# Kernel optimization log

Measured on AMD Instinct MI355X. Metric: run time of the kernel, lower is better.

The kernel has to match this reference:

```python
import jax, jax.numpy as jnp
import numpy as np
from jax import lax

D_MODEL = 256
VOCAB = 512
D_INNER = 512          # expand=2
D_STATE = 64
D_CONV = 4
HEADDIM = 32
NHEADS = D_INNER // HEADDIM  # 16
NGROUPS = 1
CHUNK = 64
D_IN_PROJ = 2 * D_INNER + 2 * NGROUPS * D_STATE + NHEADS  # 1168
CONV_DIM = D_INNER + 2 * NGROUPS * D_STATE               # 640


def setup_inputs() -> dict:
    key = jax.random.key(0)
    ks = jax.random.split(key, 8)
    B, L = 8, 4096
    input_ids = jax.random.randint(ks[0], (B, L), 0, VOCAB)
    rn = lambda k, shp, sc: (jax.random.normal(k, shp) * sc).astype(jnp.float32)
    embed_w = rn(ks[1], (VOCAB, D_MODEL), 0.02).at[0].set(0.0)  # padding_idx=0
    in_proj_w = rn(ks[2], (D_IN_PROJ, D_MODEL), D_MODEL ** -0.5)
    conv_w = rn(ks[3], (CONV_DIM, D_CONV), 0.2)
    conv_b = jnp.zeros((CONV_DIM,), jnp.float32)
    A_log = jnp.log(jax.random.uniform(ks[4], (NHEADS,), minval=1.0, maxval=16.0)).astype(jnp.float32)
    D_skip = jnp.ones((NHEADS,), jnp.float32)
    dt0 = jax.random.uniform(ks[5], (NHEADS,), minval=1e-3, maxval=0.1)
    dt_bias = jnp.log(jnp.expm1(dt0)).astype(jnp.float32)  # inverse softplus
    gate_norm_w = jnp.ones((D_INNER,), jnp.float32)
    out_proj_w = rn(ks[6], (D_MODEL, D_INNER), D_INNER ** -0.5)
    norm_w = jnp.ones((D_MODEL,), jnp.float32)
    return dict(input_ids=input_ids, embed_w=embed_w, in_proj_w=in_proj_w,
                conv_w=conv_w, conv_b=conv_b, A_log=A_log, D_skip=D_skip,
                dt_bias=dt_bias, gate_norm_w=gate_norm_w, out_proj_w=out_proj_w,
                norm_w=norm_w)


def _rmsnorm(x, w, eps):
    return x * lax.rsqrt(jnp.mean(x * x, axis=-1, keepdims=True) + eps) * w


def _segsum(a):
    # a: (..., T) -> (..., T, T); out[q,s] = sum_{s+1..q} a, -inf above diag
    T = a.shape[-1]
    c = jnp.cumsum(a, axis=-1)
    seg = c[..., :, None] - c[..., None, :]
    mask = jnp.tril(jnp.ones((T, T), bool))
    return jnp.where(mask, seg, -jnp.inf)


def _ssd(X, A, Bm, Cm):
    # X:(b,l,h,p) already *dt ; A:(b,l,h)=dt*A_head ; Bm,Cm:(b,l,n)
    b, l, h, p = X.shape
    n = Bm.shape[-1]
    c, q = l // CHUNK, CHUNK
    X = X.reshape(b, c, q, h, p)
    A = A.reshape(b, c, q, h).transpose(0, 3, 1, 2)        # (b,h,c,q)
    Bm = Bm.reshape(b, c, q, n)
    Cm = Cm.reshape(b, c, q, n)
    A_cs = jnp.cumsum(A, axis=-1)                           # (b,h,c,q)
    Lmat = jnp.exp(_segsum(A))                              # (b,h,c,q,q)
    # intra-chunk (diagonal block) output
    Y_diag = jnp.einsum('bcqn,bckn,bhcqk,bckhp->bcqhp', Cm, Bm, Lmat, X)
    # states carried to end of each chunk
    decay_states = jnp.exp(A_cs[..., -1:] - A_cs)           # (b,h,c,q)
    states = jnp.einsum('bckn,bhck,bckhp->bchpn', Bm, decay_states, X)
    chunk_decay = jnp.exp(A_cs[..., -1])                    # (b,h,c)
    def step(hprev, inp):
        dec, st = inp
        return dec[..., None, None] * hprev + st, hprev
    _, prev = lax.scan(step, jnp.zeros((b, h, p, n), X.dtype),
                       (chunk_decay.transpose(2, 0, 1), states.transpose(1, 0, 2, 3, 4)))
    prev = prev.transpose(1, 0, 2, 3, 4)                    # (b,c,h,p,n)
    Y_off = jnp.einsum('bcqn,bchpn,bhcq->bcqhp', Cm, prev, jnp.exp(A_cs))
    return (Y_diag + Y_off).reshape(b, l, h, p)


def _mamba2(u, in_proj_w, conv_w, conv_b, A_log, D_skip, dt_bias, gate_norm_w, out_proj_w):
    B, L, _ = u.shape
    zxbcdt = u @ in_proj_w.T                                # (B,L,1168)
    z = zxbcdt[..., :D_INNER]
    xBC = zxbcdt[..., D_INNER:D_INNER + CONV_DIM]
    dt = zxbcdt[..., D_INNER + CONV_DIM:]                   # (B,L,H)
    # causal depthwise conv + silu
    xBC = lax.conv_general_dilated(xBC.transpose(0, 2, 1), conv_w[:, None, :],
                                   (1,), [(D_CONV - 1, 0)],
                                   dimension_numbers=('NCH', 'OIH', 'NCH'),
                                   feature_group_count=CONV_DIM)
    xBC = jax.nn.silu(xBC + conv_b[None, :, None]).transpose(0, 2, 1)
    x = xBC[..., :D_INNER].reshape(B, L, NHEADS, HEADDIM)
    Bm = xBC[..., D_INNER:D_INNER + D_STATE]
    Cm = xBC[..., D_INNER + D_STATE:]
    dt = jax.nn.softplus(dt + dt_bias)                      # (B,L,H)
    A = -jnp.exp(A_log)                                     # (H,)
    y = _ssd(x * dt[..., None], dt * A, Bm, Cm)
    y = y + D_skip[None, None, :, None] * x
    y = y.reshape(B, L, D_INNER)
    y = _rmsnorm(y * jax.nn.silu(z), gate_norm_w, 1e-5)     # RMSNormGated
    return y @ out_proj_w.T


def reference(input_ids, embed_w, in_proj_w, conv_w, conv_b, A_log, D_skip,
              dt_bias, gate_norm_w, out_proj_w, norm_w):
    x = embed_w[input_ids]                                  # (B,L,D)
    u = _rmsnorm(x, norm_w, 1e-6)
    x = x + _mamba2(u, in_proj_w, conv_w, conv_b, A_log, D_skip,
                    dt_bias, gate_norm_w, out_proj_w)
    logits = x @ embed_w.T                                  # tied lm_head
    return logits
```

## Files before the change

kernel.cpp:

```cpp
#include <hip/hip_runtime.h>
#include <cstdint>
#include <cstddef>

#define TOK    32768
#define BATCH  8
#define SEQ    4096
#define DMODEL 256
#define DINNER 512
#define DSTATE 64
#define NH     16
#define HD     32
#define DPROJ  1168
#define NPAD   1280
#define CONVD  640
#define VOCAB  512
#define HGRP   4
#define TS     132

typedef __attribute__((ext_vector_type(8))) short bf16x8;
typedef __attribute__((ext_vector_type(4))) float f32x4;

__device__ __forceinline__ unsigned short f2bf(float f) {
    unsigned u = __float_as_uint(f);
    u += 0x7fffu + ((u >> 16) & 1u);
    return (unsigned short)(u >> 16);
}
__device__ __forceinline__ float bf2f(short s) {
    return __uint_as_float(((unsigned)(unsigned short)s) << 16);
}
__device__ __forceinline__ unsigned cvtpk(float lo, float hi) {
    unsigned r;
    asm("v_cvt_pk_bf16_f32 %0, %1, %2" : "=v"(r) : "v"(lo), "v"(hi));
    return r;
}
__device__ __forceinline__ float fsilu(float s) {
    return s * __builtin_amdgcn_rcpf(1.f + __expf(-s));
}
__device__ __forceinline__ float sp(float v) {
    return v > 20.f ? v : __logf(1.f + __expf(v));
}

__device__ __forceinline__ void gload16(const short* src, short* dst) {
    __builtin_amdgcn_global_load_lds((const __attribute__((address_space(1))) void*)src,
                                     (__attribute__((address_space(3))) void*)dst, 16, 0, 0);
}

#define U16_OFF   0
#define Z16_OFF   (U16_OFF  + (size_t)TOK*128)
#define XBC_OFF   (Z16_OFF  + (size_t)TOK*256)
#define DTS_OFF   (XBC_OFF  + (size_t)TOK*320)
#define ACS_OFF   (DTS_OFF  + (size_t)TOK*16)
#define CDEC_OFF  (ACS_OFF  + (size_t)BATCH*NH*64*64)
#define WP_OFF    (CDEC_OFF + (size_t)BATCH*NH*64)
#define WO_OFF    (WP_OFF   + 163840)
#define WE_OFF    (WO_OFF   + 65536)
#define UNION_OFF (WE_OFF   + 65536)
#define UNION_FL  ((size_t)BATCH*64*NH*2048)
#define Y16_SUB   ((size_t)TOK*256)
#define XF_SUB    ((size_t)TOK*256)
#define WS_FLOATS (UNION_OFF + UNION_FL)

__global__ void k_diag(float* out, float wsmb) {
    if (blockIdx.x == 0 && threadIdx.x == 0) out[0] = wsmb;
}

__global__ void k_cvt(const float* __restrict__ s, short* __restrict__ d, int nsrc, int ntot) {
    int i = blockIdx.x * 256 + threadIdx.x;
    if (i < ntot) d[i] = (i < nsrc) ? (short)f2bf(s[i]) : (short)0;
}

__global__ void k_embed(const int* __restrict__ ids, const float* __restrict__ embed,
                        const float* __restrict__ norm_w, short* __restrict__ u16) {
    int t = blockIdx.x;
    int lane = threadIdx.x;
    int id = ids[t];
    float4 v = ((const float4*)(embed + (size_t)id * DMODEL))[lane];
    float ss = v.x*v.x + v.y*v.y + v.z*v.z + v.w*v.w;
    #pragma unroll
    for (int o = 32; o > 0; o >>= 1) ss += __shfl_down(ss, o);
    ss = __shfl(ss, 0);
    float r = rsqrtf(ss * (1.0f / DMODEL) + 1e-6f);
    float4 w = ((const float4*)norm_w)[lane];
    unsigned p0 = cvtpk(v.x * r * w.x, v.y * r * w.y);
    unsigned p1 = cvtpk(v.z * r * w.z, v.w * r * w.w);
    ((uint2*)(u16 + (size_t)t * DMODEL))[lane] = make_uint2(p0, p1);
}

template<int MODE>
__global__ __launch_bounds__(512) void k_gemm_mfma(
    const short* __restrict__ A, const short* __restrict__ B, int K,
    float* __restrict__ outF, short* __restrict__ z16, short* __restrict__ xbc,
    float* __restrict__ dts, const float* __restrict__ dt_bias,
    const int* __restrict__ ids, const float* __restrict__ embed,
    const float* __restrict__ cw, const float* __restrict__ cb) {
    __shared__ __align__(16) short SM[32768];
    constexpr int NX = (MODE == 0) ? (NPAD / 128) : ((MODE == 1) ? (DMODEL / 128) : (VOCAB / 128));
    int tid = threadIdx.x;
    int bid = blockIdx.x;
    int slot = bid >> 3;
    int m0 = (((bid & 7) * 32) + slot / NX) << 7;
    int n0 = (slot % NX) << 7;
    int wave = tid >> 6, lane = tid & 63;
    int wm = wave >> 1, wn = wave & 1;
    int lr = lane & 15, lg = lane >> 4;
    const f32x4 zer = {0.f, 0.f, 0.f, 0.f};
    f32x4 acc[2][4];
    #pragma unroll
    for (int i = 0; i < 2; i++)
        #pragma unroll
        for (int j = 0; j < 4; j++) acc[i][j] = zer;

    const bool isXBC = (MODE == 0) && (n0 >= 512) && (n0 < 1152);
    const bool atStart = (m0 & (SEQ - 1)) == 0;
    const bool haloLane = isXBC && (wm == 0) && !atStart && (lr < 3);
    f32x4 hacc[4];
    #pragma unroll
    for (int j = 0; j < 4; j++) hacc[j] = zer;
    const bf16x8 hz = {0, 0, 0, 0, 0, 0, 0, 0};
    bf16x8 hc0 = hz, hc1 = hz, hn0 = hz, hn1 = hz;

    const int nK = K >> 6;
    const int slo = lane >> 3;
    const int skb = ((lane & 7) ^ slo) << 3;

    {
        #pragma unroll
        for (int j = 0; j < 2; j++) {
            int row = wave * 16 + j * 8 + slo;
            gload16(A + (size_t)(m0 + row) * K + skb, SM + (wave * 2 + j) * 512);
            gload16(B + (size_t)(n0 + row) * K + skb, SM + 16384 + (wave * 2 + j) * 512);
        }
        if (haloLane) {
            hc0 = *(const bf16x8*)(A + (size_t)(m0 - 3 + lr) * K + lg * 8);
            hc1 = *(const bf16x8*)(A + (size_t)(m0 - 3 + lr) * K + 32 + lg * 8);
        }
    }
    __syncthreads();

    for (int kt = 0; kt < nK; ++kt) {
        if (kt + 1 < nK) {
            int k0 = (kt + 1) << 6;
            int nb = ((kt + 1) & 1) * 8192;
            #pragma unroll
            for (int j = 0; j < 2; j++) {
                int row = wave * 16 + j * 8 + slo;
                gload16(A + (size_t)(m0 + row) * K + k0 + skb, SM + nb + (wave * 2 + j) * 512);
                gload16(B + (size_t)(n0 + row) * K + k0 + skb, SM + 16384 + nb + (wave * 2 + j) * 512);
            }
            if (haloLane) {
                hn0 = *(const bf16x8*)(A + (size_t)(m0 - 3 + lr) * K + k0 + lg * 8);
                hn1 = *(const bf16x8*)(A + (size_t)(m0 - 3 + lr) * K + k0 + 32 + lg * 8);
            }
        }
        const short* CA = SM + (kt & 1) * 8192;
        const short* CB = SM + 16384 + (kt & 1) * 8192;
        #pragma unroll
        for (int kk = 0; kk < 2; kk++) {
            int sw = (((kk << 2) + lg) ^ (lr & 7)) << 3;
            bf16x8 af[2], bfr[4];
            #pragma unroll
            for (int mi = 0; mi < 2; mi++)
                af[mi] = *(const bf16x8*)&CA[(wm * 32 + mi * 16 + lr) * 64 + sw];
            #pragma unroll
            for (int ni = 0; ni < 4; ni++)
                bfr[ni] = *(const bf16x8*)&CB[(wn * 64 + ni * 16 + lr) * 64 + sw];
            #pragma unroll
            for (int mi = 0; mi < 2; mi++)
                #pragma unroll
                for (int ni = 0; ni < 4; ni++)
                    acc[mi][ni] = __builtin_amdgcn_mfma_f32_16x16x32_bf16(af[mi], bfr[ni], acc[mi][ni], 0, 0, 0);
            if (isXBC && wm == 0) {
                bf16x8 h = (kk == 0) ? hc0 : hc1;
                #pragma unroll
                for (int ni = 0; ni < 4; ni++)
                    hacc[ni] = __builtin_amdgcn_mfma_f32_16x16x32_bf16(h, bfr[ni], hacc[ni], 0, 0, 0);
            }
        }
        __syncthreads();
        hc0 = hn0; hc1 = hn1;
    }

    if (isXBC) {
        short* Tile = SM;
        #pragma unroll
        for (int mi = 0; mi < 2; mi++)
            #pragma unroll
            for (int ni = 0; ni < 4; ni++)
                #pragma unroll
                for (int r = 0; r < 4; r++) {
                    int row = wm * 32 + mi * 16 + lg * 4 + r;
                    int col = wn * 64 + ni * 16 + lr;
                    float v = acc[mi][ni][r];
                    float vo = __shfl_xor(v, 1);
                    if (!(lr & 1))
                        *(unsigned*)&Tile[(3 + row) * TS + col] = cvtpk(v, vo);
                }
        if (wm == 0 && lg == 0) {
            #pragma unroll
            for (int ni = 0; ni < 4; ni++)
                #pragma unroll
                for (int r = 0; r < 3; r++)
                    Tile[r * TS + wn * 64 + ni * 16 + lr] = (short)f2bf(hacc[ni][r]);
        }
        __syncthreads();
        int cp = tid & 63, rg = tid >> 6;
        int colb = cp * 2;
        int ch = (n0 - 512) + colb;
        float c0w0 = cw[ch * 4], c0w1 = cw[ch * 4 + 1], c0w2 = cw[ch * 4 + 2], c0w3 = cw[ch * 4 + 3];
        float c1w0 = cw[ch * 4 + 4], c1w1 = cw[ch * 4 + 5], c1w2 = cw[ch * 4 + 6], c1w3 = cw[ch * 4 + 7];
        float b0v = cb[ch], b1v = cb[ch + 1];
        int rbase = rg * 16;
        unsigned w0 = *(const unsigned*)&Tile[(rbase + 0) * TS + colb];
        unsigned w1 = *(const unsigned*)&Tile[(rbase + 1) * TS + colb];
        unsigned w2 = *(const unsigned*)&Tile[(rbase + 2) * TS + colb];
        for (int i = 0; i < 16; i++) {
            unsigned w3 = *(const unsigned*)&Tile[(rbase + i + 3) * TS + colb];
            float s0 = b0v, s1 = b1v;
            s0 = fmaf(bf2f((short)(w0 & 0xffffu)), c0w0, s0); s1 = fmaf(bf2f((short)(w0 >> 16)), c1w0, s1);
            s0 = fmaf(bf2f((short)(w1 & 0xffffu)), c0w1, s0); s1 = fmaf(bf2f((short)(w1 >> 16)), c1w1, s1);
            s0 = fmaf(bf2f((short)(w2 & 0xffffu)), c0w2, s0); s1 = fmaf(bf2f((short)(w2 >> 16)), c1w2, s1);
            s0 = fmaf(bf2f((short)(w3 & 0xffffu)), c0w3, s0); s1 = fmaf(bf2f((short)(w3 >> 16)), c1w3, s1);
            s0 = fsilu(s0);
            s1 = fsilu(s1);
            *(unsigned*)&xbc[(size_t)(m0 + rbase + i) * CONVD + ch] = cvtpk(s0, s1);
            w0 = w1; w1 = w2; w2 = w3;
        }
        return;
    }

    #pragma unroll
    for (int mi = 0; mi < 2; mi++) {
        #pragma unroll
        for (int r = 0; r < 4; r++) {
            int row = m0 + wm * 32 + mi * 16 + lg * 4 + r;
            int id = 0;
            if (MODE == 1) id = ids[row];
            #pragma unroll
            for (int ni = 0; ni < 4; ni++) {
                int col = n0 + wn * 64 + ni * 16 + lr;
                float v = acc[mi][ni][r];
                if (MODE == 0) {
                    if (n0 < 512) {
                        float vo = __shfl_xor(v, 1);
                        if (!(lr & 1))
                            *(unsigned*)&z16[(size_t)row * DINNER + col] = cvtpk(v, vo);
                    } else if (wn == 0 && ni == 0) {
                        dts[(size_t)row * NH + lr] = sp(v + dt_bias[lr]);
                    }
                } else if (MODE == 1) {
                    float vo = __shfl_xor(v, 1);
                    if (!(lr & 1)) {
                        float2 res = *(const float2*)&embed[(size_t)id * DMODEL + col];
                        *(unsigned*)&z16[(size_t)row * DMODEL + col] = cvtpk(v + res.x, vo + res.y);
                    }
                } else {
                    outF[(size_t)row * VOCAB + col] = v;
                }
            }
        }
    }
}

__global__ __launch_bounds__(256) void k_states(const short* __restrict__ xbc, const float* __restrict__ dts,
                                                const float* __restrict__ A_log,
                                                short* __restrict__ st16,
                                                float* __restrict__ acs_g, float* __restrict__ cdec) {
    __shared__ short BsB[64 * 72];
    __shared__ short BT[64 * 72];
    __shared__ short XdS[32 * 72];
    __shared__ __align__(16) short XKP[64 * 32];
    __shared__ float dkS[HGRP][64];
    __shared__ float dtS[64];
    int tid = threadIdx.x;
    int bid = blockIdx.x;
    int hg = bid & 3;
    int bc = bid >> 2;
    int b = bc >> 6, c = bc & 63;
    int h0 = hg * HGRP;
    size_t tbase = (size_t)b * SEQ + (size_t)c * 64;
    int wave = tid >> 6, lane = tid & 63;
    int lr = lane & 15, lg = lane >> 4;

    for (int i = tid; i < 64 * 64; i += 256) {
        int q = i >> 6, n = i & 63;
        BsB[q * 72 + n] = xbc[(tbase + q) * CONVD + DINNER + n];
    }
    {
        int h = h0 + wave;
        float Ah = -__expf(A_log[h]);
        float v = dts[(tbase + lane) * NH + h] * Ah;
        #pragma unroll
        for (int off = 1; off < 64; off <<= 1) {
            float o = __shfl_up(v, off);
            if (lane >= off) v += o;
        }
        acs_g[(((size_t)(b * NH + h)) * 64 + c) * 64 + lane] = v;
        float alast = __shfl(v, 63);
        dkS[wave][lane] = __expf(alast - v);
        if (lane == 0) cdec[(b * NH + h) * 64 + c] = __expf(alast);
    }
    __syncthreads();
    for (int i = tid; i < 64 * 64; i += 256) {
        int k = i >> 6, n = i & 63;
        BT[n * 72 + k] = BsB[k * 72 + n];
    }

    for (int hh = 0; hh < HGRP; hh++) {
        int h = h0 + hh;
        {
            int s = wave * 64 + lane;
            gload16(xbc + (tbase + (s >> 2)) * CONVD + h * HD + (s & 3) * 8, XKP + wave * 512);
        }
        if (tid < 64) dtS[tid] = dts[(tbase + tid) * NH + h];
        __syncthreads();
        for (int i = tid; i < 2048; i += 256) {
            int p = i & 31, k = i >> 5;
            XdS[p * 72 + k] = (short)f2bf(bf2f(XKP[k * 32 + p]) * dtS[k] * dkS[hh][k]);
        }
        __syncthreads();
        {
            int ptile = wave & 1;
            bf16x8 a0 = *(const bf16x8*)&XdS[(ptile * 16 + lr) * 72 + lg * 8];
            bf16x8 a1 = *(const bf16x8*)&XdS[(ptile * 16 + lr) * 72 + 32 + lg * 8];
            size_t base = ((size_t)bc * NH + h) * 2048;
            #pragma unroll
            for (int j = 0; j < 2; j++) {
                int nt = (wave >> 1) * 2 + j;
                bf16x8 b0 = *(const bf16x8*)&BT[(nt * 16 + lr) * 72 + lg * 8];
                bf16x8 b1 = *(const bf16x8*)&BT[(nt * 16 + lr) * 72 + 32 + lg * 8];
                f32x4 z = {0.f, 0.f, 0.f, 0.f};
                z = __builtin_amdgcn_mfma_f32_16x16x32_bf16(a0, b0, z, 0, 0, 0);
                z = __builtin_amdgcn_mfma_f32_16x16x32_bf16(a1, b1, z, 0, 0, 0);
                #pragma unroll
                for (int r = 0; r < 4; r++) {
                    int p = ptile * 16 + lg * 4 + r;
                    float v = z[r];
                    float vo = __shfl_xor(v, 1);
                    if (!(lr & 1)) {
                        int chunk = (nt << 1) | (lr >> 3);
                        *(unsigned*)&st16[base + p * 64 + ((chunk ^ (p & 7)) << 3) + (lr & 7)] = cvtpk(v, vo);
                    }
                }
            }
        }
        __syncthreads();
    }
}

__global__ __launch_bounds__(256) void k_scan(unsigned* __restrict__ st32, const float* __restrict__ cdec) {
    int bid = blockIdx.x;
    int bh = bid >> 2, seg = bid & 3;
    int b = bh >> 4, h = bh & 15;
    int off = seg * 256 + threadIdx.x;
    float p0 = 0.f, p1 = 0.f;
    for (int c = 0; c < 64; c++) {
        float dec = cdec[bh * 64 + c];
        size_t idx = ((((size_t)b * 64 + c) * NH) + h) * 1024 + off;
        unsigned v = st32[idx];
        float s0 = bf2f((short)(v & 0xffffu));
        float s1 = bf2f((short)(v >> 16));
        st32[idx] = cvtpk(p0, p1);
        p0 = fmaf(dec, p0, s0);
        p1 = fmaf(dec, p1, s1);
    }
}

__global__ __launch_bounds__(256) void k_y(const short* __restrict__ xbc, const float* __restrict__ dts,
                                           const short* __restrict__ st16, const float* __restrict__ acs_g,
                                           const float* __restrict__ D_skip, short* __restrict__ Y16) {
    __shared__ short CsB[64 * 72];
    __shared__ short Wsh[64 * 72];
    __shared__ short XtS[32 * 72];
    __shared__ __align__(16) short PtL[32 * 64];
    __shared__ __align__(16) short XKP[64 * 32];
    __shared__ float acsH[64];
    __shared__ float dtS[64];
    int tid = threadIdx.x;
    int bid = blockIdx.x;
    int hg = bid & 3;
    int bc = bid >> 2;
    int b = bc >> 6, c = bc & 63;
    int h0 = hg * HGRP;
    size_t tbase = (size_t)b * SEQ + (size_t)c * 64;
    int wave = tid >> 6, lane = tid & 63;
    int lr = lane & 15, lg = lane >> 4;

    for (int i = tid; i < 64 * 64; i += 256) {
        int q = i >> 6, n = i & 63;
        const short* rowp = xbc + (tbase + q) * CONVD + DINNER;
        Wsh[q * 72 + n] = rowp[n];
        CsB[q * 72 + n] = rowp[DSTATE + n];
    }
    __syncthreads();

    f32x4 macc[4];
    bf16x8 ca0 = *(const bf16x8*)&CsB[(wave * 16 + lr) * 72 + lg * 8];
    bf16x8 ca1 = *(const bf16x8*)&CsB[(wave * 16 + lr) * 72 + 32 + lg * 8];
    {
        #pragma unroll
        for (int ct = 0; ct < 4; ct++) {
            bf16x8 b0 = *(const bf16x8*)&Wsh[(ct * 16 + lr) * 72 + lg * 8];
            bf16x8 b1 = *(const bf16x8*)&Wsh[(ct * 16 + lr) * 72 + 32 + lg * 8];
            f32x4 z = {0.f, 0.f, 0.f, 0.f};
            z = __builtin_amdgcn_mfma_f32_16x16x32_bf16(ca0, b0, z, 0, 0, 0);
            z = __builtin_amdgcn_mfma_f32_16x16x32_bf16(ca1, b1, z, 0, 0, 0);
            macc[ct] = z;
        }
    }
    __syncthreads();

    for (int hh = 0; hh < HGRP; hh++) {
        int h = h0 + hh;
        {
            int s = wave * 64 + lane;
            gload16(xbc + (tbase + (s >> 2)) * CONVD + h * HD + (s & 3) * 8, XKP + wave * 512);
            gload16(st16 + ((size_t)bc * NH + h) * 2048 + s * 8, PtL + wave * 512);
        }
        if (tid < 64) {
            acsH[tid] = acs_g[(((size_t)(b * NH + h)) * 64 + c) * 64 + tid];
            dtS[tid] = dts[(tbase + tid) * NH + h];
        }
        __syncthreads();
        #pragma unroll
        for (int ct = 0; ct < 4; ct++) {
            int k = ct * 16 + lr;
            #pragma unroll
            for (int r = 0; r < 4; r++) {
                int q = wave * 16 + lg * 4 + r;
                float wv = 0.f;
                if (k <= q) wv = macc[ct][r] * __expf(acsH[q] - acsH[k]);
                float wo = __shfl_xor(wv, 1);
                if (!(lr & 1))
                    *(unsigned*)&Wsh[q * 72 + k] = cvtpk(wv, wo);
            }
        }
        for (int i = tid; i < 2048; i += 256) {
            int p = i & 31, k = i >> 5;
            XtS[p * 72 + k] = (short)f2bf(bf2f(XKP[k * 32 + p]) * dtS[k]);
        }
        __syncthreads();
        float eq[4];
        #pragma unroll
        for (int r = 0; r < 4; r++) eq[r] = __expf(acsH[wave * 16 + lg * 4 + r]);
        float dsk = D_skip[h];
        bf16x8 wa0 = *(const bf16x8*)&Wsh[(wave * 16 + lr) * 72 + lg * 8];
        bf16x8 wa1 = *(const bf16x8*)&Wsh[(wave * 16 + lr) * 72 + 32 + lg * 8];
        #pragma unroll
        for (int pt = 0; pt < 2; pt++) {
            int p = pt * 16 + lr;
            bf16x8 xb0 = *(const bf16x8*)&XtS[p * 72 + lg * 8];
            bf16x8 xb1 = *(const bf16x8*)&XtS[p * 72 + 32 + lg * 8];
            f32x4 zd = {0.f, 0.f, 0.f, 0.f};
            zd = __builtin_amdgcn_mfma_f32_16x16x32_bf16(wa0, xb0, zd, 0, 0, 0);
            zd = __builtin_amdgcn_mfma_f32_16x16x32_bf16(wa1, xb1, zd, 0, 0, 0);
            bf16x8 pb0 = *(const bf16x8*)&PtL[p * 64 + ((lg ^ (p & 7)) << 3)];
            bf16x8 pb1 = *(const bf16x8*)&PtL[p * 64 + (((lg + 4) ^ (p & 7)) << 3)];
            f32x4 zo = {0.f, 0.f, 0.f, 0.f};
            zo = __builtin_amdgcn_mfma_f32_16x16x32_bf16(ca0, pb0, zo, 0, 0, 0);
            zo = __builtin_amdgcn_mfma_f32_16x16x32_bf16(ca1, pb1, zo, 0, 0, 0);
            #pragma unroll
            for (int r = 0; r < 4; r++) {
                int q = wave * 16 + lg * 4 + r;
                float xv = bf2f(XKP[q * 32 + p]);
                float v = zd[r] + eq[r] * zo[r] + dsk * xv;
                float vo = __shfl_xor(v, 1);
                if (!(lr & 1))
                    *(unsigned*)&Y16[((tbase + q) * NH + h) * HD + p] = cvtpk(v, vo);
            }
        }
        __syncthreads();
    }
}

__global__ void k_gate(const short* __restrict__ Y16, const short* __restrict__ z16,
                       const float* __restrict__ gw, short* __restrict__ Yb) {
    int t = blockIdx.x;
    int lane = threadIdx.x;
    union { int4 v; short s[8]; } zu, yu;
    zu.v = *(const int4*)(z16 + (size_t)t * DINNER + lane * 8);
    yu.v = *(const int4*)(Y16 + (size_t)t * DINNER + lane * 8);
    float g[8];
    float ss = 0.f;
    #pragma unroll
    for (int i = 0; i < 8; i++) {
        float zf = bf2f(zu.s[i]);
        g[i] = bf2f(yu.s[i]) * fsilu(zf);
        ss += g[i] * g[i];
    }
    #pragma unroll
    for (int o = 32; o > 0; o >>= 1) ss += __shfl_down(ss, o);
    ss = __shfl(ss, 0);
    float rr = rsqrtf(ss * (1.0f / DINNER) + 1e-5f);
    const float* wr = gw + lane * 8;
    float4 w0 = *(const float4*)wr;
    float4 w1 = *(const float4*)(wr + 4);
    float wv[8] = {w0.x, w0.y, w0.z, w0.w, w1.x, w1.y, w1.z, w1.w};
    union { uint4 v; unsigned u[4]; } ou;
    #pragma unroll
    for (int i = 0; i < 4; i++)
        ou.u[i] = cvtpk(g[2*i] * rr * wv[2*i], g[2*i+1] * rr * wv[2*i+1]);
    *(uint4*)(Yb + (size_t)t * DINNER + lane * 8) = ou.v;
}

extern "C" void kernel_launch(void* const* d_in, const int* in_sizes, int n_in,
                              void* d_out, int out_size, void* d_ws, size_t ws_size,
                              hipStream_t stream) {
    const int*   ids        = (const int*)d_in[0];
    const float* embed_w    = (const float*)d_in[1];
    const float* in_proj_w  = (const float*)d_in[2];
    const float* conv_w     = (const float*)d_in[3];
    const float* conv_b     = (const float*)d_in[4];
    const float* A_log      = (const float*)d_in[5];
    const float* D_skip     = (const float*)d_in[6];
    const float* dt_bias    = (const float*)d_in[7];
    const float* gate_w     = (const float*)d_in[8];
    const float* out_proj_w = (const float*)d_in[9];
    const float* norm_w     = (const float*)d_in[10];
    float* out = (float*)d_out;

    if (ws_size < WS_FLOATS * sizeof(float)) {
        k_diag<<<1, 64, 0, stream>>>(out, (float)(ws_size >> 20));
        return;
    }

    float* ws   = (float*)d_ws;
    short* u16  = (short*)(ws + U16_OFF);
    short* z16  = (short*)(ws + Z16_OFF);
    short* xbc  = (short*)(ws + XBC_OFF);
    float* dts  = ws + DTS_OFF;
    float* acs  = ws + ACS_OFF;
    float* cdec = ws + CDEC_OFF;
    short* Wp   = (short*)(ws + WP_OFF);
    short* Wo   = (short*)(ws + WO_OFF);
    short* We   = (short*)(ws + WE_OFF);
    short* st16 = (short*)(ws + UNION_OFF);
    short* Y16  = (short*)(ws + UNION_OFF + Y16_SUB);
    short* Yb   = (short*)(ws + UNION_OFF);
    short* xf16 = (short*)(ws + UNION_OFF + XF_SUB);

    k_cvt<<<(NPAD * DMODEL + 255) / 256, 256, 0, stream>>>(in_proj_w, Wp, DPROJ * DMODEL, NPAD * DMODEL);
    k_cvt<<<(DMODEL * DINNER + 255) / 256, 256, 0, stream>>>(out_proj_w, Wo, DMODEL * DINNER, DMODEL * DINNER);
    k_cvt<<<(VOCAB * DMODEL + 255) / 256, 256, 0, stream>>>(embed_w, We, VOCAB * DMODEL, VOCAB * DMODEL);
    k_embed<<<TOK, 64, 0, stream>>>(ids, embed_w, norm_w, u16);
    k_gemm_mfma<0><<<(NPAD / 128) * 256, 512, 0, stream>>>(
        u16, Wp, DMODEL, nullptr, z16, xbc, dts, dt_bias, nullptr, nullptr, conv_w, conv_b);
    k_states<<<BATCH * 64 * 4, 256, 0, stream>>>(xbc, dts, A_log, st16, acs, cdec);
    k_scan<<<BATCH * NH * 4, 256, 0, stream>>>((unsigned*)st16, cdec);
    k_y<<<BATCH * 64 * 4, 256, 0, stream>>>(xbc, dts, st16, acs, D_skip, Y16);
    k_gate<<<TOK, 64, 0, stream>>>(Y16, z16, gate_w, Yb);
    k_gemm_mfma<1><<<(DMODEL / 128) * 256, 512, 0, stream>>>(
        Yb, Wo, DINNER, nullptr, xf16, nullptr, nullptr, nullptr, ids, embed_w, nullptr, nullptr);
    k_gemm_mfma<2><<<(VOCAB / 128) * 256, 512, 0, stream>>>(
        xf16, We, DMODEL, out, nullptr, nullptr, nullptr, nullptr, nullptr, nullptr, nullptr, nullptr);
}
```

Before: 224.2 us.

## Fuse gated RMSNorm into out-projection GEMM and fold gate weight into Wo

Removes the separate k_gate kernel. The new k_outproj computes y*silu(z) on the fly while loading the A tile, accumulates the row sum of squares, and applies the RMS scale in the epilogue. The gate norm weight is folded into the bf16 out_proj weights during conversion. This avoids writing and re-reading the gated activation (32K x 512 bf16) and one launch. In exchange, each of the two N-tile blocks per row block recomputes the gate and global-loads Y and z without the async LDS path, and there is no double buffering.

```diff
diff --git a/kernel.cpp b/kernel.cpp
--- a/kernel.cpp
+++ b/kernel.cpp
@@ -57,7 +57,6 @@
 #define UNION_OFF (WE_OFF   + 65536)
 #define UNION_FL  ((size_t)BATCH*64*NH*2048)
 #define Y16_SUB   ((size_t)TOK*256)
-#define XF_SUB    ((size_t)TOK*256)
 #define WS_FLOATS (UNION_OFF + UNION_FL)
 
 __global__ void k_diag(float* out, float wsmb) {
@@ -67,6 +66,11 @@
 __global__ void k_cvt(const float* __restrict__ s, short* __restrict__ d, int nsrc, int ntot) {
     int i = blockIdx.x * 256 + threadIdx.x;
     if (i < ntot) d[i] = (i < nsrc) ? (short)f2bf(s[i]) : (short)0;
+}
+__global__ void k_cvt_gate(const float* __restrict__ s, const float* __restrict__ gw,
+                           short* __restrict__ d, int ntot) {
+    int i = blockIdx.x * 256 + threadIdx.x;
+    if (i < ntot) d[i] = (short)f2bf(s[i] * gw[i & (DINNER - 1)]);
 }
 
 __global__ void k_embed(const int* __restrict__ ids, const float* __restrict__ embed,
@@ -91,10 +95,9 @@
     const short* __restrict__ A, const short* __restrict__ B, int K,
     float* __restrict__ outF, short* __restrict__ z16, short* __restrict__ xbc,
     float* __restrict__ dts, const float* __restrict__ dt_bias,
-    const int* __restrict__ ids, const float* __restrict__ embed,
     const float* __restrict__ cw, const float* __restrict__ cb) {
     __shared__ __align__(16) short SM[32768];
-    constexpr int NX = (MODE == 0) ? (NPAD / 128) : ((MODE == 1) ? (DMODEL / 128) : (VOCAB / 128));
+    constexpr int NX = (MODE == 0) ? (NPAD / 128) : (VOCAB / 128);
     int tid = threadIdx.x;
     int bid = blockIdx.x;
     int slot = bid >> 3;
@@ -233,8 +236,6 @@
         #pragma unroll
         for (int r = 0; r < 4; r++) {
             int row = m0 + wm * 32 + mi * 16 + lg * 4 + r;
-            int id = 0;
-            if (MODE == 1) id = ids[row];
             #pragma unroll
             for (int ni = 0; ni < 4; ni++) {
                 int col = n0 + wn * 64 + ni * 16 + lr;
@@ -247,14 +248,112 @@
                     } else if (wn == 0 && ni == 0) {
                         dts[(size_t)row * NH + lr] = sp(v + dt_bias[lr]);
                     }
-                } else if (MODE == 1) {
-                    float vo = __shfl_xor(v, 1);
-                    if (!(lr & 1)) {
-                        float2 res = *(const float2*)&embed[(size_t)id * DMODEL + col];
-                        *(unsigned*)&z16[(size_t)row * DMODEL + col] = cvtpk(v + res.x, vo + res.y);
-                    }
                 } else {
                     outF[(size_t)row * VOCAB + col] = v;
+                }
+            }
+        }
+    }
+}
+
+__global__ __launch_bounds__(512) void k_outproj(
+    const short* __restrict__ Y16, const short* __restrict__ z16,
+    const short* __restrict__ Wo, const int* __restrict__ ids,
+    const float* __restrict__ embed, short* __restrict__ xf16) {
+    __shared__ __align__(16) short As[8192];
+    __shared__ __align__(16) short Bs[8192];
+    __shared__ float rmsS[128];
+    int tid = threadIdx.x;
+    int bid = blockIdx.x;
+    int slot = bid >> 3;
+    int m0 = (((bid & 7) * 32) + (slot >> 1)) << 7;
+    int n0 = (slot & 1) << 7;
+    int wave = tid >> 6, lane = tid & 63;
+    int wm = wave >> 1, wn = wave & 1;
+    int lr = lane & 15, lg = lane >> 4;
+    const f32x4 zer = {0.f, 0.f, 0.f, 0.f};
+    f32x4 acc[2][4];
+    #pragma unroll
+    for (int i = 0; i < 2; i++)
+        #pragma unroll
+        for (int j = 0; j < 4; j++) acc[i][j] = zer;
+
+    const int arow = tid >> 2;
+    const int ac0 = (tid & 3) * 2;
+    const int slo = lane >> 3;
+    const int skb = ((lane & 7) ^ slo) << 3;
+    float ssq = 0.f;
+
+    for (int kt = 0; kt < 8; ++kt) {
+        int k0 = kt << 6;
+        #pragma unroll
+        for (int j = 0; j < 2; j++) {
+            int row = wave * 16 + j * 8 + slo;
+            gload16(Wo + (size_t)(n0 + row) * DINNER + k0 + skb, Bs + (wave * 2 + j) * 512);
+        }
+        union { int4 v; short s[8]; } y0u, y1u, z0u, z1u;
+        const size_t rbase = (size_t)(m0 + arow) * DINNER + k0 + ac0 * 8;
+        y0u.v = *(const int4*)(Y16 + rbase);
+        y1u.v = *(const int4*)(Y16 + rbase + 8);
+        z0u.v = *(const int4*)(z16 + rbase);
+        z1u.v = *(const int4*)(z16 + rbase + 8);
+        unsigned pk[8];
+        #pragma unroll
+        for (int e = 0; e < 4; e++) {
+            float g0 = bf2f(y0u.s[2*e])     * fsilu(bf2f(z0u.s[2*e]));
+            float g1 = bf2f(y0u.s[2*e + 1]) * fsilu(bf2f(z0u.s[2*e + 1]));
+            ssq += g0 * g0 + g1 * g1;
+            pk[e] = cvtpk(g0, g1);
+        }
+        #pragma unroll
+        for (int e = 0; e < 4; e++) {
+            float g0 = bf2f(y1u.s[2*e])     * fsilu(bf2f(z1u.s[2*e]));
+            float g1 = bf2f(y1u.s[2*e + 1]) * fsilu(bf2f(z1u.s[2*e + 1]));
+            ssq += g0 * g0 + g1 * g1;
+            pk[4 + e] = cvtpk(g0, g1);
+        }
+        *(int4*)&As[arow * 64 + ((ac0 ^ (arow & 7)) << 3)] = *(int4*)&pk[0];
+        *(int4*)&As[arow * 64 + (((ac0 + 1) ^ (arow & 7)) << 3)] = *(int4*)&pk[4];
+        __syncthreads();
+        #pragma unroll
+        for (int kk = 0; kk < 2; kk++) {
+            int sw = (((kk << 2) + lg) ^ (lr & 7)) << 3;
+            bf16x8 af[2], bfr[4];
+            #pragma unroll
+            for (int mi = 0; mi < 2; mi++)
+                af[mi] = *(const bf16x8*)&As[(wm * 32 + mi * 16 + lr) * 64 + sw];
+            #pragma unroll
+            for (int ni = 0; ni < 4; ni++)
+                bfr[ni] = *(const bf16x8*)&Bs[(wn * 64 + ni * 16 + lr) * 64 + sw];
+            #pragma unroll
+            for (int mi = 0; mi < 2; mi++)
+                #pragma unroll
+                for (int ni = 0; ni < 4; ni++)
+                    acc[mi][ni] = __builtin_amdgcn_mfma_f32_16x16x32_bf16(af[mi], bfr[ni], acc[mi][ni], 0, 0, 0);
+        }
+        __syncthreads();
+    }
+    ssq += __shfl_xor(ssq, 1);
+    ssq += __shfl_xor(ssq, 2);
+    if ((tid & 3) == 0) rmsS[arow] = rsqrtf(ssq * (1.0f / DINNER) + 1e-5f);
+    __syncthreads();
+
+    #pragma unroll
+    for (int mi = 0; mi < 2; mi++) {
+        #pragma unroll
+        for (int r = 0; r < 4; r++) {
+            int rl = wm * 32 + mi * 16 + lg * 4 + r;
+            int row = m0 + rl;
+            int id = ids[row];
+            float rm = rmsS[rl];
+            #pragma unroll
+            for (int ni = 0; ni < 4; ni++) {
+                int col = n0 + wn * 64 + ni * 16 + lr;
+                float v = acc[mi][ni][r] * rm;
+                float vo = __shfl_xor(v, 1);
+                if (!(lr & 1)) {
+                    float2 res = *(const float2*)&embed[(size_t)id * DMODEL + col];
+                    *(unsigned*)&xf16[(size_t)row * DMODEL + col] = cvtpk(v + res.x, vo + res.y);
                 }
             }
         }
@@ -472,36 +571,6 @@
     }
 }
 
-__global__ void k_gate(const short* __restrict__ Y16, const short* __restrict__ z16,
-                       const float* __restrict__ gw, short* __restrict__ Yb) {
-    int t = blockIdx.x;
-    int lane = threadIdx.x;
-    union { int4 v; short s[8]; } zu, yu;
-    zu.v = *(const int4*)(z16 + (size_t)t * DINNER + lane * 8);
-    yu.v = *(const int4*)(Y16 + (size_t)t * DINNER + lane * 8);
-    float g[8];
-    float ss = 0.f;
-    #pragma unroll
-    for (int i = 0; i < 8; i++) {
-        float zf = bf2f(zu.s[i]);
-        g[i] = bf2f(yu.s[i]) * fsilu(zf);
-        ss += g[i] * g[i];
-    }
-    #pragma unroll
-    for (int o = 32; o > 0; o >>= 1) ss += __shfl_down(ss, o);
-    ss = __shfl(ss, 0);
-    float rr = rsqrtf(ss * (1.0f / DINNER) + 1e-5f);
-    const float* wr = gw + lane * 8;
-    float4 w0 = *(const float4*)wr;
-    float4 w1 = *(const float4*)(wr + 4);
-    float wv[8] = {w0.x, w0.y, w0.z, w0.w, w1.x, w1.y, w1.z, w1.w};
-    union { uint4 v; unsigned u[4]; } ou;
-    #pragma unroll
-    for (int i = 0; i < 4; i++)
-        ou.u[i] = cvtpk(g[2*i] * rr * wv[2*i], g[2*i+1] * rr * wv[2*i+1]);
-    *(uint4*)(Yb + (size_t)t * DINNER + lane * 8) = ou.v;
-}
-
 extern "C" void kernel_launch(void* const* d_in, const int* in_sizes, int n_in,
                               void* d_out, int out_size, void* d_ws, size_t ws_size,
                               hipStream_t stream) {
@@ -535,21 +604,18 @@
     short* We   = (short*)(ws + WE_OFF);
     short* st16 = (short*)(ws + UNION_OFF);
     short* Y16  = (short*)(ws + UNION_OFF + Y16_SUB);
-    short* Yb   = (short*)(ws + UNION_OFF);
-    short* xf16 = (short*)(ws + UNION_OFF + XF_SUB);
+    short* xf16 = (short*)(ws + UNION_OFF);
 
     k_cvt<<<(NPAD * DMODEL + 255) / 256, 256, 0, stream>>>(in_proj_w, Wp, DPROJ * DMODEL, NPAD * DMODEL);
-    k_cvt<<<(DMODEL * DINNER + 255) / 256, 256, 0, stream>>>(out_proj_w, Wo, DMODEL * DINNER, DMODEL * DINNER);
+    k_cvt_gate<<<(DMODEL * DINNER + 255) / 256, 256, 0, stream>>>(out_proj_w, gate_w, Wo, DMODEL * DINNER);
     k_cvt<<<(VOCAB * DMODEL + 255) / 256, 256, 0, stream>>>(embed_w, We, VOCAB * DMODEL, VOCAB * DMODEL);
     k_embed<<<TOK, 64, 0, stream>>>(ids, embed_w, norm_w, u16);
     k_gemm_mfma<0><<<(NPAD / 128) * 256, 512, 0, stream>>>(
-        u16, Wp, DMODEL, nullptr, z16, xbc, dts, dt_bias, nullptr, nullptr, conv_w, conv_b);
+        u16, Wp, DMODEL, nullptr, z16, xbc, dts, dt_bias, conv_w, conv_b);
     k_states<<<BATCH * 64 * 4, 256, 0, stream>>>(xbc, dts, A_log, st16, acs, cdec);
     k_scan<<<BATCH * NH * 4, 256, 0, stream>>>((unsigned*)st16, cdec);
     k_y<<<BATCH * 64 * 4, 256, 0, stream>>>(xbc, dts, st16, acs, D_skip, Y16);
-    k_gate<<<TOK, 64, 0, stream>>>(Y16, z16, gate_w, Yb);
-    k_gemm_mfma<1><<<(DMODEL / 128) * 256, 512, 0, stream>>>(
-        Yb, Wo, DINNER, nullptr, xf16, nullptr, nullptr, nullptr, ids, embed_w, nullptr, nullptr);
+    k_outproj<<<(DMODEL / 128) * 256, 512, 0, stream>>>(Y16, z16, Wo, ids, embed_w, xf16);
     k_gemm_mfma<2><<<(VOCAB / 128) * 256, 512, 0, stream>>>(
-        xf16, We, DMODEL, out, nullptr, nullptr, nullptr, nullptr, nullptr, nullptr, nullptr, nullptr);
-}
+        xf16, We, DMODEL, out, nullptr, nullptr, nullptr, nullptr, nullptr, nullptr);
+}
```

New measurement: 220.4 us. No clear change (-1.7%).
